# Optimization experiments

Measured on AMD Instinct MI355X. Metric: run time of the kernel, lower is better.

Reference implementation:

```python
import jax, jax.numpy as jnp
import numpy as np

EPS = 1e-6
N_HEADS = 16


def _stable_softmax(x):
    # max subtracted with stop_gradient (torch .detach()), clamp to [-50, 50], eps in denom
    x_max = jax.lax.stop_gradient(jnp.max(x, axis=-1, keepdims=True))
    exp_x = jnp.exp(jnp.clip(x - x_max, -50.0, 50.0))
    return exp_x / (jnp.sum(exp_x, axis=-1, keepdims=True) + EPS)


def setup_inputs() -> dict:
    key = jax.random.key(0)
    k1, k2, k3 = jax.random.split(key, 3)
    B, S, D = 2, 2048, 1024
    x = jax.random.normal(k1, (B, S, D), dtype=jnp.float32)
    Wqkv = jax.random.normal(k2, (3 * D, D), dtype=jnp.float32) * 0.02
    Wout = jax.random.normal(k3, (D, D), dtype=jnp.float32) * (0.02 / np.sqrt(2))
    return {"x": x, "Wqkv": Wqkv, "Wout": Wout}


def reference(x, Wqkv, Wout):
    B, S, D = x.shape
    H = N_HEADS
    Dh = D // H
    scale = 1.0 / np.sqrt(Dh)
    # qkv projection (torch Linear: x @ W.T), split into q,k,v -> (B,H,S,Dh)
    qkv = (x @ Wqkv.T).reshape(B, S, 3, H, Dh)
    qkv = jnp.transpose(qkv, (2, 0, 3, 1, 4))
    q, k, v = qkv[0], qkv[1], qkv[2]
    # chunked attention is mathematically identical to full attention here
    scores = jnp.einsum('bhqd,bhkd->bhqk', q, k) * scale
    attn = _stable_softmax(scores)
    out = jnp.einsum('bhqk,bhkd->bhqd', attn, v)  # (B,H,S,Dh)
    out = jnp.transpose(out, (0, 2, 1, 3)).reshape(B, S, D)
    return out @ Wout.T
```

## Files before the change

kernel.cpp:

```cpp
#include <hip/hip_runtime.h>
#include <hip/hip_bf16.h>
#include <stdint.h>

#define S_LEN   2048
#define D_MODEL 1024
#define NH      16
#define DH      64
#define BATCH   2
#define TOKENS  (BATCH * S_LEN)

typedef __bf16 bf16;
typedef __bf16 bf16x8 __attribute__((ext_vector_type(8)));
typedef __bf16 b16x4  __attribute__((ext_vector_type(4)));
typedef float  f32x4  __attribute__((ext_vector_type(4)));

__device__ __forceinline__ void async_lds16(const void* g, void* l) {
  __builtin_amdgcn_global_load_lds((__attribute__((address_space(1))) void*)g,
                                   (__attribute__((address_space(3))) void*)l,
                                   16, 0, 0);
}

__global__ __launch_bounds__(256) void convert_kernel(
    const float* __restrict__ src, bf16* __restrict__ dst, int n8) {
  const int i = blockIdx.x * 256 + threadIdx.x;
  if (i >= n8) return;
  const f32x4 a = *(const f32x4*)(src + (size_t)i * 8);
  const f32x4 b = *(const f32x4*)(src + (size_t)i * 8 + 4);
  bf16x8 o;
#pragma unroll
  for (int j = 0; j < 4; j++) { o[j] = (bf16)a[j]; o[j + 4] = (bf16)b[j]; }
  *(bf16x8*)(dst + (size_t)i * 8) = o;
}

#define BM 128
#define BN 128
#define BK 32

#define GEMM_CORE(APTR, BPTR, KDIM)                                              \
  __shared__ __align__(16) bf16 As[BM * BK];                                     \
  __shared__ __align__(16) bf16 Bs[BN * BK];                                     \
  const int tid  = threadIdx.x;                                                  \
  const int wave = tid >> 6, lane = tid & 63;                                    \
  const int quad = lane >> 4, l16 = lane & 15;                                   \
  const int m0 = blockIdx.y * BM;                                                \
  const int n0 = blockIdx.x * BN;                                                \
  const int wm = (wave >> 1) * 64, wn = (wave & 1) * 64;                         \
  f32x4 acc[4][4] = {};                                                          \
  const int c0 = tid, c1 = tid + 256;                                            \
  for (int k0 = 0; k0 < (KDIM); k0 += BK) {                                      \
    async_lds16((APTR) + (size_t)(m0 + (c0 >> 2)) * (KDIM) + k0 + (c0 & 3) * 8,  \
                As + c0 * 8);                                                    \
    async_lds16((APTR) + (size_t)(m0 + (c1 >> 2)) * (KDIM) + k0 + (c1 & 3) * 8,  \
                As + c1 * 8);                                                    \
    async_lds16((BPTR) + (size_t)(n0 + (c0 >> 2)) * (KDIM) + k0 + (c0 & 3) * 8,  \
                Bs + c0 * 8);                                                    \
    async_lds16((BPTR) + (size_t)(n0 + (c1 >> 2)) * (KDIM) + k0 + (c1 & 3) * 8,  \
                Bs + c1 * 8);                                                    \
    __syncthreads();                                                             \
    bf16x8 af[4], bfr[4];                                                        \
    _Pragma("unroll") for (int i = 0; i < 4; i++)                                \
        af[i] = *(const bf16x8*)(As + (wm + i * 16 + l16) * BK + quad * 8);      \
    _Pragma("unroll") for (int j = 0; j < 4; j++)                                \
        bfr[j] = *(const bf16x8*)(Bs + (wn + j * 16 + l16) * BK + quad * 8);     \
    _Pragma("unroll") for (int i = 0; i < 4; i++)                                \
      _Pragma("unroll") for (int j = 0; j < 4; j++)                              \
        acc[i][j] = __builtin_amdgcn_mfma_f32_16x16x32_bf16(af[i], bfr[j],       \
                                                            acc[i][j], 0, 0, 0); \
    __syncthreads();                                                             \
  }

__global__ __launch_bounds__(256) void gemm_qkv_kernel(
    const bf16* __restrict__ X, const bf16* __restrict__ W,
    bf16* __restrict__ Qo, bf16* __restrict__ Ko, bf16* __restrict__ VTo) {
  GEMM_CORE(X, W, D_MODEL)
  const int t = n0 >> 10;
#pragma unroll
  for (int i = 0; i < 4; i++) {
    const int rowb = m0 + wm + i * 16 + quad * 4;
    const int b = rowb >> 11, s0 = rowb & 2047;
#pragma unroll
    for (int j = 0; j < 4; j++) {
      const int col = n0 + wn + j * 16 + l16;
      const int h = (col >> 6) & 15, d = col & 63;
      if (t == 2) {
        b16x4 v4;
#pragma unroll
        for (int r = 0; r < 4; r++) v4[r] = (bf16)acc[i][j][r];
        *(b16x4*)(VTo + ((size_t)(b * NH + h) * DH + d) * S_LEN + s0) = v4;
      } else {
#pragma unroll
        for (int r = 0; r < 4; r++) {
          const float v = acc[i][j][r];
          if (t == 0)
            Qo[((size_t)(b * NH + h) * S_LEN + s0 + r) * DH + d] = (bf16)(v * 0.125f);
          else
            Ko[((size_t)(b * NH + h) * S_LEN + s0 + r) * DH + d] = (bf16)v;
        }
      }
    }
  }
}

__global__ __launch_bounds__(256) void gemm_out_kernel(
    const bf16* __restrict__ A, const bf16* __restrict__ W,
    float* __restrict__ Out) {
  GEMM_CORE(A, W, D_MODEL)
#pragma unroll
  for (int i = 0; i < 4; i++) {
    const int rowb = m0 + wm + i * 16 + quad * 4;
#pragma unroll
    for (int j = 0; j < 4; j++) {
      const int col = n0 + wn + j * 16 + l16;
#pragma unroll
      for (int r = 0; r < 4; r++)
        Out[(size_t)(rowb + r) * D_MODEL + col] = acc[i][j][r];
    }
  }
}

#define AKS 72
#define AVS 72
#define PTS 72

__global__ __launch_bounds__(512) void attn_kernel(
    const bf16* __restrict__ Q, const bf16* __restrict__ K,
    const bf16* __restrict__ VT, bf16* __restrict__ AO) {
  __shared__ __align__(16) bf16 Ks[64 * AKS];
  __shared__ __align__(16) bf16 Vs[64 * AVS];
  __shared__ __align__(16) bf16 PT[8 * 16 * PTS];

  const int tid  = threadIdx.x;
  const int wave = tid >> 6, lane = tid & 63;
  const int quad = lane >> 4, l16 = lane & 15;
  const int qb = blockIdx.x & 15;
  const int bh = blockIdx.x >> 4;
  const bf16* qp = Q  + (size_t)bh * S_LEN * DH;
  const bf16* kp = K  + (size_t)bh * S_LEN * DH;
  const bf16* vp = VT + (size_t)bh * DH * S_LEN;
  const int qr0 = qb * 128 + wave * 16;

  const bf16x8 aq0 = *(const bf16x8*)(qp + (size_t)(qr0 + l16) * DH + quad * 8);
  const bf16x8 aq1 = *(const bf16x8*)(qp + (size_t)(qr0 + l16) * DH + 32 + quad * 8);

  f32x4 oT[4] = {};
  float lsum = 0.f;
  bf16* PTw = PT + wave * (16 * PTS);

  const int rc = tid >> 3, kc = (tid & 7) * 8;

  bf16x8 kv = *(const bf16x8*)(kp + (size_t)rc * DH + kc);
  bf16x8 vv = *(const bf16x8*)(vp + (size_t)rc * S_LEN + kc);

  for (int kb = 0; kb < S_LEN / 64; kb++) {
    __syncthreads();
    *(bf16x8*)(Ks + rc * AKS + kc) = kv;
    *(bf16x8*)(Vs + rc * AVS + kc) = vv;
    __syncthreads();

    const int kn = (kb + 1 < S_LEN / 64) ? kb + 1 : kb;
    kv = *(const bf16x8*)(kp + (size_t)(kn * 64 + rc) * DH + kc);
    vv = *(const bf16x8*)(vp + (size_t)rc * S_LEN + kn * 64 + kc);

#pragma unroll
    for (int t = 0; t < 4; t++) {
      const bf16x8 ak0 = *(const bf16x8*)(Ks + (t * 16 + l16) * AKS + quad * 8);
      const bf16x8 ak1 = *(const bf16x8*)(Ks + (t * 16 + l16) * AKS + 32 + quad * 8);
      f32x4 st = {};
      st = __builtin_amdgcn_mfma_f32_16x16x32_bf16(ak0, aq0, st, 0, 0, 0);
      st = __builtin_amdgcn_mfma_f32_16x16x32_bf16(ak1, aq1, st, 0, 0, 0);
      b16x4 pb;
      float ls = 0.f;
#pragma unroll
      for (int r = 0; r < 4; r++) {
        const float e = __expf(st[r]);
        ls += e;
        pb[r] = (bf16)e;
      }
      lsum += ls;
      *(b16x4*)(PTw + l16 * PTS + t * 16 + quad * 4) = pb;
    }

#pragma unroll
    for (int c = 0; c < 2; c++) {
      const bf16x8 pf = *(const bf16x8*)(PTw + l16 * PTS + c * 32 + quad * 8);
#pragma unroll
      for (int nt = 0; nt < 4; nt++) {
        const bf16x8 av =
            *(const bf16x8*)(Vs + (nt * 16 + l16) * AVS + c * 32 + quad * 8);
        oT[nt] = __builtin_amdgcn_mfma_f32_16x16x32_bf16(av, pf, oT[nt], 0, 0, 0);
      }
    }
  }

  lsum += __shfl_xor(lsum, 16);
  lsum += __shfl_xor(lsum, 32);
  const float inv = 1.0f / (lsum + 1e-6f);

  const int b = bh >> 4, h = bh & 15;
  const int srow = qr0 + l16;
  const size_t base = (size_t)(b * S_LEN + srow) * D_MODEL + h * DH;
#pragma unroll
  for (int nt = 0; nt < 4; nt++) {
    b16x4 o4;
#pragma unroll
    for (int r = 0; r < 4; r++) o4[r] = (bf16)(oT[nt][r] * inv);
    *(b16x4*)(AO + base + nt * 16 + quad * 4) = o4;
  }
}

extern "C" void kernel_launch(void* const* d_in, const int* in_sizes, int n_in,
                              void* d_out, int out_size, void* d_ws, size_t ws_size,
                              hipStream_t stream) {
  const float* x    = (const float*)d_in[0];
  const float* wqkv = (const float*)d_in[1];
  const float* wout = (const float*)d_in[2];
  float* out = (float*)d_out;

  bf16* Q  = (bf16*)d_ws;
  bf16* K  = Q  + (size_t)TOKENS * D_MODEL;
  bf16* VT = K  + (size_t)TOKENS * D_MODEL;
  bf16* xb = VT + (size_t)TOKENS * D_MODEL;
  bf16* AO = xb;
  bf16* wqkvb = (bf16*)d_out;
  bf16* woutb = Q;

  convert_kernel<<<dim3(TOKENS * D_MODEL / (256 * 8)), dim3(256), 0, stream>>>(
      x, xb, TOKENS * D_MODEL / 8);
  convert_kernel<<<dim3(3 * D_MODEL * D_MODEL / (256 * 8)), dim3(256), 0, stream>>>(
      wqkv, wqkvb, 3 * D_MODEL * D_MODEL / 8);

  gemm_qkv_kernel<<<dim3(3 * D_MODEL / BN, TOKENS / BM), dim3(256), 0, stream>>>(
      xb, wqkvb, Q, K, VT);

  attn_kernel<<<dim3(BATCH * NH * (S_LEN / 128)), dim3(512), 0, stream>>>(Q, K, VT, AO);

  convert_kernel<<<dim3(D_MODEL * D_MODEL / (256 * 8)), dim3(256), 0, stream>>>(
      wout, woutb, D_MODEL * D_MODEL / 8);

  gemm_out_kernel<<<dim3(D_MODEL / BN, TOKENS / BM), dim3(256), 0, stream>>>(
      AO, woutb, out);
}
```

Before: 197.8 us.

## Fuse input conversions, shrink attention and output GEMM tiles for more blocks

```diff
diff --git a/kernel.cpp b/kernel.cpp
--- a/kernel.cpp
+++ b/kernel.cpp
@@ -20,16 +20,27 @@
                                    16, 0, 0);
 }
 
+__device__ __forceinline__ void conv8(const float* src, bf16* dst, int i) {
+  const f32x4 a = *(const f32x4*)(src + (size_t)i * 8);
+  const f32x4 b = *(const f32x4*)(src + (size_t)i * 8 + 4);
+  bf16x8 o;
+#pragma unroll
+  for (int j = 0; j < 4; j++) { o[j] = (bf16)a[j]; o[j + 4] = (bf16)b[j]; }
+  *(bf16x8*)(dst + (size_t)i * 8) = o;
+}
+
+__global__ __launch_bounds__(256) void convert2_kernel(
+    const float* __restrict__ s0, bf16* __restrict__ d0, int n0_,
+    const float* __restrict__ s1, bf16* __restrict__ d1, int n1_) {
+  const int i = blockIdx.x * 256 + threadIdx.x;
+  if (i < n0_) conv8(s0, d0, i);
+  else if (i - n0_ < n1_) conv8(s1, d1, i - n0_);
+}
+
 __global__ __launch_bounds__(256) void convert_kernel(
     const float* __restrict__ src, bf16* __restrict__ dst, int n8) {
   const int i = blockIdx.x * 256 + threadIdx.x;
-  if (i >= n8) return;
-  const f32x4 a = *(const f32x4*)(src + (size_t)i * 8);
-  const f32x4 b = *(const f32x4*)(src + (size_t)i * 8 + 4);
-  bf16x8 o;
-#pragma unroll
-  for (int j = 0; j < 4; j++) { o[j] = (bf16)a[j]; o[j + 4] = (bf16)b[j]; }
-  *(bf16x8*)(dst + (size_t)i * 8) = o;
+  if (i < n8) conv8(src, dst, i);
 }
 
 #define BM 128
@@ -104,9 +115,41 @@
 __global__ __launch_bounds__(256) void gemm_out_kernel(
     const bf16* __restrict__ A, const bf16* __restrict__ W,
     float* __restrict__ Out) {
-  GEMM_CORE(A, W, D_MODEL)
-#pragma unroll
-  for (int i = 0; i < 4; i++) {
+  __shared__ __align__(16) bf16 As[64 * BK];
+  __shared__ __align__(16) bf16 Bs[128 * BK];
+  const int tid  = threadIdx.x;
+  const int wave = tid >> 6, lane = tid & 63;
+  const int quad = lane >> 4, l16 = lane & 15;
+  const int m0 = blockIdx.y * 64;
+  const int n0 = blockIdx.x * 128;
+  const int wm = (wave >> 1) * 32, wn = (wave & 1) * 64;
+  f32x4 acc[2][4] = {};
+  const int c0 = tid, c1 = tid + 256;
+  for (int k0 = 0; k0 < D_MODEL; k0 += BK) {
+    async_lds16(A + (size_t)(m0 + (c0 >> 2)) * D_MODEL + k0 + (c0 & 3) * 8,
+                As + c0 * 8);
+    async_lds16(W + (size_t)(n0 + (c0 >> 2)) * D_MODEL + k0 + (c0 & 3) * 8,
+                Bs + c0 * 8);
+    async_lds16(W + (size_t)(n0 + (c1 >> 2)) * D_MODEL + k0 + (c1 & 3) * 8,
+                Bs + c1 * 8);
+    __syncthreads();
+    bf16x8 af[2], bfr[4];
+#pragma unroll
+    for (int i = 0; i < 2; i++)
+      af[i] = *(const bf16x8*)(As + (wm + i * 16 + l16) * BK + quad * 8);
+#pragma unroll
+    for (int j = 0; j < 4; j++)
+      bfr[j] = *(const bf16x8*)(Bs + (wn + j * 16 + l16) * BK + quad * 8);
+#pragma unroll
+    for (int i = 0; i < 2; i++)
+#pragma unroll
+      for (int j = 0; j < 4; j++)
+        acc[i][j] = __builtin_amdgcn_mfma_f32_16x16x32_bf16(af[i], bfr[j],
+                                                            acc[i][j], 0, 0, 0);
+    __syncthreads();
+  }
+#pragma unroll
+  for (int i = 0; i < 2; i++) {
     const int rowb = m0 + wm + i * 16 + quad * 4;
 #pragma unroll
     for (int j = 0; j < 4; j++) {
@@ -122,22 +165,22 @@
 #define AVS 72
 #define PTS 72
 
-__global__ __launch_bounds__(512) void attn_kernel(
+__global__ __launch_bounds__(256) void attn_kernel(
     const bf16* __restrict__ Q, const bf16* __restrict__ K,
     const bf16* __restrict__ VT, bf16* __restrict__ AO) {
   __shared__ __align__(16) bf16 Ks[64 * AKS];
   __shared__ __align__(16) bf16 Vs[64 * AVS];
-  __shared__ __align__(16) bf16 PT[8 * 16 * PTS];
+  __shared__ __align__(16) bf16 PT[4 * 16 * PTS];
 
   const int tid  = threadIdx.x;
   const int wave = tid >> 6, lane = tid & 63;
   const int quad = lane >> 4, l16 = lane & 15;
-  const int qb = blockIdx.x & 15;
-  const int bh = blockIdx.x >> 4;
+  const int qb = blockIdx.x & 31;
+  const int bh = blockIdx.x >> 5;
   const bf16* qp = Q  + (size_t)bh * S_LEN * DH;
   const bf16* kp = K  + (size_t)bh * S_LEN * DH;
   const bf16* vp = VT + (size_t)bh * DH * S_LEN;
-  const int qr0 = qb * 128 + wave * 16;
+  const int qr0 = qb * 64 + wave * 16;
 
   const bf16x8 aq0 = *(const bf16x8*)(qp + (size_t)(qr0 + l16) * DH + quad * 8);
   const bf16x8 aq1 = *(const bf16x8*)(qp + (size_t)(qr0 + l16) * DH + 32 + quad * 8);
@@ -146,20 +189,26 @@
   float lsum = 0.f;
   bf16* PTw = PT + wave * (16 * PTS);
 
-  const int rc = tid >> 3, kc = (tid & 7) * 8;
-
-  bf16x8 kv = *(const bf16x8*)(kp + (size_t)rc * DH + kc);
-  bf16x8 vv = *(const bf16x8*)(vp + (size_t)rc * S_LEN + kc);
+  const int rc0 = tid >> 3, rc1 = rc0 + 32, kc = (tid & 7) * 8;
+
+  bf16x8 kv0 = *(const bf16x8*)(kp + (size_t)rc0 * DH + kc);
+  bf16x8 kv1 = *(const bf16x8*)(kp + (size_t)rc1 * DH + kc);
+  bf16x8 vv0 = *(const bf16x8*)(vp + (size_t)rc0 * S_LEN + kc);
+  bf16x8 vv1 = *(const bf16x8*)(vp + (size_t)rc1 * S_LEN + kc);
 
   for (int kb = 0; kb < S_LEN / 64; kb++) {
     __syncthreads();
-    *(bf16x8*)(Ks + rc * AKS + kc) = kv;
-    *(bf16x8*)(Vs + rc * AVS + kc) = vv;
+    *(bf16x8*)(Ks + rc0 * AKS + kc) = kv0;
+    *(bf16x8*)(Ks + rc1 * AKS + kc) = kv1;
+    *(bf16x8*)(Vs + rc0 * AVS + kc) = vv0;
+    *(bf16x8*)(Vs + rc1 * AVS + kc) = vv1;
     __syncthreads();
 
     const int kn = (kb + 1 < S_LEN / 64) ? kb + 1 : kb;
-    kv = *(const bf16x8*)(kp + (size_t)(kn * 64 + rc) * DH + kc);
-    vv = *(const bf16x8*)(vp + (size_t)rc * S_LEN + kn * 64 + kc);
+    kv0 = *(const bf16x8*)(kp + (size_t)(kn * 64 + rc0) * DH + kc);
+    kv1 = *(const bf16x8*)(kp + (size_t)(kn * 64 + rc1) * DH + kc);
+    vv0 = *(const bf16x8*)(vp + (size_t)rc0 * S_LEN + kn * 64 + kc);
+    vv1 = *(const bf16x8*)(vp + (size_t)rc1 * S_LEN + kn * 64 + kc);
 
 #pragma unroll
     for (int t = 0; t < 4; t++) {
@@ -224,19 +273,19 @@
   bf16* wqkvb = (bf16*)d_out;
   bf16* woutb = Q;
 
-  convert_kernel<<<dim3(TOKENS * D_MODEL / (256 * 8)), dim3(256), 0, stream>>>(
-      x, xb, TOKENS * D_MODEL / 8);
-  convert_kernel<<<dim3(3 * D_MODEL * D_MODEL / (256 * 8)), dim3(256), 0, stream>>>(
-      wqkv, wqkvb, 3 * D_MODEL * D_MODEL / 8);
+  const int nx8 = TOKENS * D_MODEL / 8;
+  const int nw8 = 3 * D_MODEL * D_MODEL / 8;
+  convert2_kernel<<<dim3((nx8 + nw8 + 255) / 256), dim3(256), 0, stream>>>(
+      x, xb, nx8, wqkv, wqkvb, nw8);
 
   gemm_qkv_kernel<<<dim3(3 * D_MODEL / BN, TOKENS / BM), dim3(256), 0, stream>>>(
       xb, wqkvb, Q, K, VT);
 
-  attn_kernel<<<dim3(BATCH * NH * (S_LEN / 128)), dim3(512), 0, stream>>>(Q, K, VT, AO);
+  attn_kernel<<<dim3(BATCH * NH * (S_LEN / 64)), dim3(256), 0, stream>>>(Q, K, VT, AO);
 
   convert_kernel<<<dim3(D_MODEL * D_MODEL / (256 * 8)), dim3(256), 0, stream>>>(
       wout, woutb, D_MODEL * D_MODEL / 8);
 
-  gemm_out_kernel<<<dim3(D_MODEL / BN, TOKENS / BM), dim3(256), 0, stream>>>(
+  gemm_out_kernel<<<dim3(D_MODEL / 128, TOKENS / 64), dim3(256), 0, stream>>>(
       AO, woutb, out);
 }
```

New measurement: 201.8 us. 2.0% more time.
